# Kernel tuning notes

Measured on AMD Instinct MI355X. Metric: run time of the kernel, lower is better.

## Reference

```python
import jax, jax.numpy as jnp
import numpy as np

D_MODEL = 768
N_LAYER = 8
EXPAND = 2
D_INNER = EXPAND * D_MODEL          # 1536
HEADDIM = 64
NHEADS = D_INNER // HEADDIM         # 24
D_STATE = 128
D_CONV = 4
NGROUPS = 1
CONV_DIM = D_INNER + 2 * NGROUPS * D_STATE      # 1792
D_IN_PROJ = 2 * D_INNER + 2 * NGROUPS * D_STATE + NHEADS  # 3352
DIM_INP = 6
DIM_OUT = 5
BATCH = 4
SEQ = 2048
EPS = 1e-5


def rmsnorm(x, w):
    return x * jax.lax.rsqrt(jnp.mean(x * x, axis=-1, keepdims=True) + EPS) * w


def setup_inputs() -> dict:
    key = jax.random.key(0)
    ks = jax.random.split(key, 12)
    nrm = lambda k, shape, s=0.02: jax.random.normal(k, shape, jnp.float32) * s
    x = jax.random.normal(ks[0], (BATCH, SEQ, DIM_INP), jnp.float32)
    y = jax.random.normal(ks[1], (BATCH, SEQ, DIM_OUT), jnp.float32)
    W_emb = nrm(ks[2], (D_MODEL, DIM_INP))
    b_emb = jnp.zeros((D_MODEL,), jnp.float32)
    # stacked per-layer Mamba2 params
    W_in = nrm(ks[3], (N_LAYER, D_IN_PROJ, D_MODEL))
    conv_w = nrm(ks[4], (N_LAYER, CONV_DIM, D_CONV), 0.2)
    conv_b = jnp.zeros((N_LAYER, CONV_DIM), jnp.float32)
    dt0 = jax.random.uniform(ks[5], (N_LAYER, NHEADS), jnp.float32, 1e-3, 1e-1)
    dt_bias = jnp.log(jnp.expm1(dt0))  # inverse softplus of target dt
    A_log = jnp.log(jax.random.uniform(ks[6], (N_LAYER, NHEADS), jnp.float32, 1.0, 16.0))
    Dp = jnp.ones((N_LAYER, NHEADS), jnp.float32)
    norm_w = jnp.ones((N_LAYER, D_INNER), jnp.float32)     # gated RMSNorm inside Mamba2
    W_out = nrm(ks[7], (N_LAYER, D_MODEL, D_INNER))
    block_norm_w = jnp.ones((N_LAYER, D_MODEL), jnp.float32)  # prenorm RMSNorm per block
    norm_f_w = jnp.ones((D_MODEL,), jnp.float32)
    W_head = nrm(ks[8], (DIM_OUT, D_MODEL))
    return dict(x=x, y=y, W_emb=W_emb, b_emb=b_emb, W_in=W_in, conv_w=conv_w,
                conv_b=conv_b, dt_bias=dt_bias, A_log=A_log, Dp=Dp, norm_w=norm_w,
                W_out=W_out, block_norm_w=block_norm_w, norm_f_w=norm_f_w, W_head=W_head)


def _mamba2(u, W_in_l, conv_w_l, conv_b_l, dt_bias_l, A_log_l, D_l, norm_w_l, W_out_l):
    B, L, _ = u.shape
    zxbcdt = jnp.einsum('bld,ed->ble', u, W_in_l)  # [B,L,D_IN_PROJ]
    z = zxbcdt[..., :D_INNER]
    xBC = zxbcdt[..., D_INNER:D_INNER + CONV_DIM]
    dt = jax.nn.softplus(zxbcdt[..., D_INNER + CONV_DIM:] + dt_bias_l)  # [B,L,H]
    # causal depthwise conv1d, kernel D_CONV
    xp = jnp.pad(xBC, ((0, 0), (D_CONV - 1, 0), (0, 0)))
    xBC = sum(xp[:, k:k + L, :] * conv_w_l[:, k] for k in range(D_CONV)) + conv_b_l
    xBC = jax.nn.silu(xBC)
    xh = xBC[..., :D_INNER].reshape(B, L, NHEADS, HEADDIM)
    Bm = xBC[..., D_INNER:D_INNER + D_STATE]   # [B,L,N] (ngroups=1)
    Cm = xBC[..., D_INNER + D_STATE:]          # [B,L,N]
    A = -jnp.exp(A_log_l)                       # [H]
    decay = jnp.exp(dt * A)                     # [B,L,H]
    dtx = dt[..., None] * xh                    # [B,L,H,P]

    def step(h, inp):
        dec_t, dtx_t, B_t, C_t = inp            # [B,H],[B,H,P],[B,N],[B,N]
        h = h * dec_t[..., None, None] + dtx_t[..., None] * B_t[:, None, None, :]
        y_t = jnp.einsum('bhpn,bn->bhp', h, C_t)
        return h, y_t

    h0 = jnp.zeros((B, NHEADS, HEADDIM, D_STATE), u.dtype)
    _, ys = jax.lax.scan(step, h0, (decay.transpose(1, 0, 2), dtx.transpose(1, 0, 2, 3),
                                    Bm.transpose(1, 0, 2), Cm.transpose(1, 0, 2)))
    ys = ys.transpose(1, 0, 2, 3) + xh * D_l[None, None, :, None]  # skip term D*x
    yf = ys.reshape(B, L, D_INNER)
    yf = rmsnorm(yf * jax.nn.silu(z), norm_w_l)  # gated RMSNorm (norm_before_gate=False)
    return jnp.einsum('bld,ed->ble', yf, W_out_l)


def _forward(x, W_emb, b_emb, W_in, conv_w, conv_b, dt_bias, A_log, Dp, norm_w,
             W_out, block_norm_w, norm_f_w, W_head):
    h = jnp.einsum('bli,di->bld', x, W_emb) + b_emb
    res = jnp.zeros_like(h)

    def layer_step(carry, lp):
        h, res = carry
        Wi, cw, cb, dtb, Al, Dl, nw, Wo, bnw = lp
        res = h + res
        hn = rmsnorm(res, bnw)
        h = _mamba2(hn, Wi, cw, cb, dtb, Al, Dl, nw, Wo)
        return (h, res), None

    (h, res), _ = jax.lax.scan(layer_step, (h, res),
                               (W_in, conv_w, conv_b, dt_bias, A_log, Dp, norm_w, W_out, block_norm_w))
    res = h + res
    hn = rmsnorm(res, norm_f_w)
    return jnp.einsum('bld,od->blo', hn, W_head)


def reference(x, y, W_emb, b_emb, W_in, conv_w, conv_b, dt_bias, A_log, Dp, norm_w,
              W_out, block_norm_w, norm_f_w, W_head):
    out = _forward(x, W_emb, b_emb, W_in, conv_w, conv_b, dt_bias, A_log, Dp, norm_w,
                   W_out, block_norm_w, norm_f_w, W_head)
    loss = jnp.mean((out - y) ** 2)
    return out, loss
```

## Files before the change

### kernel.cpp

```cpp
#include <hip/hip_runtime.h>
#include <hip/hip_bf16.h>
#include <math.h>

#define BATCH 4
#define SEQ 2048
#define DMODEL 768
#define NLAYER 8
#define DINNER 1536
#define HEADDIM 64
#define NHEADS 24
#define DSTATE 128
#define CONVDIM 1792
#define DINPROJ 3352
#define NPAD 3456
#define NPADW 3584
#define ROWS (BATCH*SEQ)
#define EPS 1e-5f
#define QCH 128
#define NCH (SEQ/QCH)

typedef __bf16 bf16;
typedef bf16 bf16x8 __attribute__((ext_vector_type(8)));
typedef bf16 bf16x4 __attribute__((ext_vector_type(4)));
typedef float f32x4 __attribute__((ext_vector_type(4)));

#define GLD(src, dst) __builtin_amdgcn_global_load_lds( \
    (const __attribute__((address_space(1))) void*)(src), \
    (__attribute__((address_space(3))) void*)(dst), 16, 0, 0)

__device__ __forceinline__ void bar_sync() {
    asm volatile("" ::: "memory");
    __builtin_amdgcn_s_barrier();
    asm volatile("" ::: "memory");
}

__device__ __forceinline__ float fsilu(float x) { return x / (1.f + __expf(-x)); }

__global__ void k_embed(const float* __restrict__ x, const float* __restrict__ We,
                        const float* __restrict__ be, float* __restrict__ res) {
    int idx = blockIdx.x * 256 + threadIdx.x;
    int d0 = (idx % (DMODEL / 4)) * 4;
    int bl = idx / (DMODEL / 4);
    float xv[6];
#pragma unroll
    for (int i = 0; i < 6; ++i) xv[i] = x[bl * 6 + i];
    float4 o;
    float* op = &o.x;
#pragma unroll
    for (int j = 0; j < 4; ++j) {
        float acc = be[d0 + j];
#pragma unroll
        for (int i = 0; i < 6; ++i) acc += xv[i] * We[(d0 + j) * 6 + i];
        op[j] = acc;
    }
    *(float4*)(res + (long)bl * DMODEL + d0) = o;
}

__global__ __launch_bounds__(192) void k_rmsnorm(const float* __restrict__ res,
                                                 const float* __restrict__ w,
                                                 bf16* __restrict__ out) {
    __shared__ float sm[3];
    int r = blockIdx.x, tid = threadIdx.x;
    int d0 = tid * 4;
    float4 v = *(const float4*)(res + (long)r * DMODEL + d0);
    float ss = v.x * v.x + v.y * v.y + v.z * v.z + v.w * v.w;
#pragma unroll
    for (int off = 32; off; off >>= 1) ss += __shfl_down(ss, off, 64);
    if ((tid & 63) == 0) sm[tid >> 6] = ss;
    __syncthreads();
    float sc = rsqrtf((sm[0] + sm[1] + sm[2]) / (float)DMODEL + EPS);
    float4 wv = *(const float4*)(w + d0);
    bf16x4 o;
    o[0] = (bf16)(v.x * sc * wv.x);
    o[1] = (bf16)(v.y * sc * wv.y);
    o[2] = (bf16)(v.z * sc * wv.z);
    o[3] = (bf16)(v.w * sc * wv.w);
    *(bf16x4*)(out + (long)r * DMODEL + d0) = o;
}

__global__ void k_cvt_in(const float* __restrict__ src, bf16* __restrict__ dst) {
    long e = ((long)blockIdx.x * 256 + threadIdx.x) * 4;
    int l = (int)(e / (NPADW * DMODEL));
    long rem = e % (NPADW * DMODEL);
    int n = (int)(rem / DMODEL);
    int d = (int)(rem % DMODEL);
    bf16x4 o;
    if (n < DINPROJ) {
        float4 v = *(const float4*)(src + ((long)l * DINPROJ + n) * DMODEL + d);
        o[0] = (bf16)v.x; o[1] = (bf16)v.y; o[2] = (bf16)v.z; o[3] = (bf16)v.w;
    } else {
        o[0] = (bf16)0.f; o[1] = (bf16)0.f; o[2] = (bf16)0.f; o[3] = (bf16)0.f;
    }
    *(bf16x4*)(dst + e) = o;
}
__global__ void k_cvt_out(const float* __restrict__ src, bf16* __restrict__ dst) {
    long e = ((long)blockIdx.x * 256 + threadIdx.x) * 4;
    float4 v = *(const float4*)(src + e);
    bf16x4 o;
    o[0] = (bf16)v.x; o[1] = (bf16)v.y; o[2] = (bf16)v.z; o[3] = (bf16)v.w;
    *(bf16x4*)(dst + e) = o;
}

template <typename OT, int BM, int BN, int TH, bool ACC>
__global__ __launch_bounds__(TH) void k_gemm(const bf16* __restrict__ A, const bf16* __restrict__ B,
                                             OT* __restrict__ C, int K, int ldc, int Nact) {
    constexpr int NW  = TH / 64;
    constexpr int nWn = (BN / 64 < 4) ? BN / 64 : 4;
    constexpr int nWm = NW / nWn;
    constexpr int WMR = BM / nWm;
    constexpr int MI  = WMR / 16;
    constexpr int MH  = MI / 2;
    constexpr int NI  = 4;
    constexpr int RG  = TH / 8;
    constexpr int AG  = BM / RG;
    constexpr int BG  = BN / RG;
    __shared__ bf16 As[2][BM * 64];
    __shared__ bf16 Bs[2][BN * 64];
    const int tid = threadIdx.x;
    const int lane = tid & 63;
    const int w = tid >> 6;
    const int wm = w / nWn, wn = w % nWn;
    const long rowA0 = (long)blockIdx.x * BM;
    const long rowB0 = (long)blockIdx.y * BN;
    const int srow = tid >> 3;
    const int scol = ((tid & 7) ^ (srow & 7)) * 8;
    const bf16* Ab = A + rowA0 * K + scol;
    const bf16* Bb = B + rowB0 * K + scol;

    f32x4 acc[MI][NI];
    const f32x4 vz = {0.f, 0.f, 0.f, 0.f};
#pragma unroll
    for (int mi = 0; mi < MI; ++mi)
#pragma unroll
        for (int ni = 0; ni < NI; ++ni) acc[mi][ni] = vz;

    auto stage = [&](int buf, int kt) {
#pragma unroll
        for (int j = 0; j < AG; ++j)
            GLD(Ab + (long)(j * RG + srow) * K + kt, &As[buf][(j * TH + w * 64) * 8]);
#pragma unroll
        for (int j = 0; j < BG; ++j)
            GLD(Bb + (long)(j * RG + srow) * K + kt, &Bs[buf][(j * TH + w * 64) * 8]);
    };
    auto waitv = [&]() {
        if constexpr (AG + BG == 8) asm volatile("s_waitcnt vmcnt(8)" ::: "memory");
        else                        asm volatile("s_waitcnt vmcnt(6)" ::: "memory");
    };

    bf16x8 bfr[NI][2];
    bf16x8 af[MH][2];
    auto rd_bfr = [&](int buf) {
        const char* BsB = (const char*)Bs[buf];
#pragma unroll
        for (int ni = 0; ni < NI; ++ni)
#pragma unroll
            for (int ks = 0; ks < 2; ++ks) {
                int r = wn * 64 + ni * 16 + (lane & 15);
                bfr[ni][ks] = *(const bf16x8*)(BsB + r * 128 + ((ks * 64 + (lane >> 4) * 16) ^ ((r & 7) << 4)));
            }
    };
    auto rd_af = [&](int buf, int m0) {
        const char* AsB = (const char*)As[buf];
#pragma unroll
        for (int mi = 0; mi < MH; ++mi)
#pragma unroll
            for (int ks = 0; ks < 2; ++ks) {
                int r = wm * WMR + (m0 + mi) * 16 + (lane & 15);
                af[mi][ks] = *(const bf16x8*)(AsB + r * 128 + ((ks * 64 + (lane >> 4) * 16) ^ ((r & 7) << 4)));
            }
    };
    auto do_half = [&](int m0) {
#pragma unroll
        for (int mi = 0; mi < MH; ++mi)
#pragma unroll
            for (int ni = 0; ni < NI; ++ni)
#pragma unroll
                for (int ks = 0; ks < 2; ++ks)
                    acc[m0 + mi][ni] = __builtin_amdgcn_mfma_f32_16x16x32_bf16(af[mi][ks], bfr[ni][ks], acc[m0 + mi][ni], 0, 0, 0);
    };

    const int NT = K / 64;
    stage(0, 0);
    stage(1, 64);
    for (int t = 0; t < NT - 2; ++t) {
        waitv();
        bar_sync();
        rd_bfr(t & 1);
        rd_af(t & 1, 0);
        do_half(0);
        rd_af(t & 1, MH);
        asm volatile("s_waitcnt lgkmcnt(0)" ::: "memory");
        bar_sync();
        stage(t & 1, (t + 2) * 64);
        __builtin_amdgcn_sched_barrier(0);
        do_half(MH);
    }
    {
        waitv();
        bar_sync();
        rd_bfr((NT - 2) & 1);
        rd_af((NT - 2) & 1, 0);
        do_half(0);
        rd_af((NT - 2) & 1, MH);
        do_half(MH);
    }
    {
        asm volatile("s_waitcnt vmcnt(0)" ::: "memory");
        bar_sync();
        rd_bfr((NT - 1) & 1);
        rd_af((NT - 1) & 1, 0);
        do_half(0);
        rd_af((NT - 1) & 1, MH);
        do_half(MH);
    }

    const int crow = (lane >> 4) * 4;
    const int ccol = lane & 15;
#pragma unroll
    for (int mi = 0; mi < MI; ++mi)
#pragma unroll
        for (int ni = 0; ni < NI; ++ni) {
            long r0 = rowA0 + wm * WMR + mi * 16 + crow;
            long c0 = rowB0 + wn * 64 + ni * 16 + ccol;
            if ((int)c0 < Nact) {
#pragma unroll
                for (int j = 0; j < 4; ++j) {
                    if constexpr (ACC) C[(r0 + j) * ldc + c0] += (OT)acc[mi][ni][j];
                    else               C[(r0 + j) * ldc + c0]  = (OT)acc[mi][ni][j];
                }
            }
        }
}

__global__ void k_convBC(const bf16* __restrict__ zx, const float* __restrict__ cw,
                         const float* __restrict__ cb, bf16* __restrict__ bc) {
    int idx = blockIdx.x * 256 + threadIdx.x;
    int c8 = idx & 31; int blt = idx >> 5;
    int t = blt % SEQ;
    int ch = DINNER + c8 * 8;
    long bbase = (long)(blt - t) * NPAD;
    float cwa[8][4];
#pragma unroll
    for (int j = 0; j < 8; ++j) {
        float4 tv = *(const float4*)(cw + (ch + j) * 4);
        cwa[j][0] = tv.x; cwa[j][1] = tv.y; cwa[j][2] = tv.z; cwa[j][3] = tv.w;
    }
    float acc[8];
#pragma unroll
    for (int j = 0; j < 8; ++j) acc[j] = cb[ch + j];
#pragma unroll
    for (int k = 0; k < 4; ++k) {
        int tt = t + k - 3;
        if (tt >= 0) {
            bf16x8 v = *(const bf16x8*)(zx + bbase + (long)tt * NPAD + DINNER + ch);
#pragma unroll
            for (int j = 0; j < 8; ++j) acc[j] += (float)v[j] * cwa[j][k];
        }
    }
    bf16x8 o;
#pragma unroll
    for (int j = 0; j < 8; ++j) o[j] = (bf16)fsilu(acc[j]);
    *(bf16x8*)(bc + (long)blt * 256 + c8 * 8) = o;
}

__global__ __launch_bounds__(256) void k_prepL(const bf16* __restrict__ zx, const bf16* __restrict__ bc,
                                               const float* __restrict__ cw_l, const float* __restrict__ cb_l,
                                               const float* __restrict__ dt_bias_l,
                                               const float* __restrict__ Alog,
                                               float* __restrict__ Sarr, float* __restrict__ dtc,
                                               float* __restrict__ Pcb,
                                               bf16* __restrict__ XT, bf16* __restrict__ Lbuf) {
    __shared__ float S_lds[128], wl_lds[128], wtot[2];
    __shared__ bf16 Xs[136 * 64];
    __shared__ bf16 Xw[64 * 128];
    __shared__ bf16 Bt[128 * 128];
    int blk = blockIdx.x;
    int b = blk / (NHEADS * NCH);
    int r = blk % (NHEADS * NCH);
    int h = r / NCH;
    int c = r % NCH;
    int tid = threadIdx.x, lane = tid & 63, wid = tid >> 6;
    long brow0 = (long)b * SEQ + c * QCH;
#pragma unroll
    for (int i = 0; i < 5; ++i) {
        int base = i * 256 + wid * 64;
        if (base < 1048) {
            int idx = base + lane;
            long g = brow0 - 3 + (idx >> 3);
            if (g < 0) g = 0;
            if (g > (long)ROWS - 1) g = (long)ROWS - 1;
            GLD(zx + g * NPAD + DINNER + h * HEADDIM + (idx & 7) * 8,
                (char*)Xs + (long)base * 16);
        }
    }
    float ps = 0.f, dtv = 0.f;
    if (tid < 128) {
        float raw = (float)zx[(brow0 + tid) * NPAD + DINNER + CONVDIM + h] + dt_bias_l[h];
        dtv = (raw > 15.f) ? raw : log1pf(__expf(raw));
        float Ah = -__expf(Alog[h]);
        ps = dtv * Ah;
#pragma unroll
        for (int off = 1; off < 64; off <<= 1) {
            float o = __shfl_up(ps, off, 64);
            if ((tid & 63) >= off) ps += o;
        }
        if ((tid & 63) == 63) wtot[tid >> 6] = ps;
    }
    __syncthreads();
    if (tid < 128) {
        if (tid >= 64) ps += wtot[0];
        S_lds[tid] = ps;
    }
    __syncthreads();
    float Sl = S_lds[127];
    if (tid < 128) {
        wl_lds[tid] = __expf(Sl - ps) * dtv;
        Sarr[blk * QCH + tid] = ps;
        dtc[blk * QCH + tid] = dtv;
        if (tid == 127) Pcb[blk] = __expf(Sl);
    }
    __syncthreads();
    {
        int p = tid >> 2, q = tid & 3;
        float4 cwv = *(const float4*)(cw_l + (h * HEADDIM + p) * 4);
        float cbv = cb_l[h * HEADDIM + p];
        float cwa[4] = {cwv.x, cwv.y, cwv.z, cwv.w};
        char* xtb = (char*)XT + (((long)blk) << 14);
#pragma unroll
        for (int ub = 0; ub < 4; ++ub) {
            int u0 = q * 32 + ub * 8;
            bf16x8 vx, vw;
#pragma unroll
            for (int k = 0; k < 8; ++k) {
                int u = u0 + k;
                float a = cbv;
#pragma unroll
                for (int tt = 0; tt < 4; ++tt) {
                    if (c > 0 || u + tt >= 3)
                        a += (float)Xs[(u + tt) * 64 + p] * cwa[tt];
                }
                bf16 xb = (bf16)fsilu(a);
                vx[k] = xb;
                vw[k] = (bf16)((float)xb * wl_lds[u]);
            }
            long off = (long)((p * 256 + u0 * 2) ^ ((p & 7) << 4));
            *(bf16x8*)(xtb + off) = vx;
            *(bf16x8*)((char*)Xw + off) = vw;
        }
    }
#pragma unroll
    for (int nb = 0; nb < 2; ++nb) {
        __syncthreads();
#pragma unroll
        for (int i = 0; i < 4; ++i) {
            int idx = i * 256 + tid;
            GLD(bc + (brow0 + (idx >> 3)) * 256 + nb * 64 + (idx & 7) * 8,
                (char*)Xs + (i * 256 + wid * 64) * 16);
        }
        __syncthreads();
        int nl = tid >> 2, q = tid & 3;
        int n = nb * 64 + nl;
#pragma unroll
        for (int ub = 0; ub < 4; ++ub) {
            int u0 = q * 32 + ub * 8;
            bf16x8 v;
#pragma unroll
            for (int k = 0; k < 8; ++k) v[k] = Xs[(u0 + k) * 64 + nl];
            long off = (long)((n * 256 + u0 * 2) ^ ((n & 7) << 4));
            *(bf16x8*)((char*)Bt + off) = v;
        }
    }
    __syncthreads();
    f32x4 acc[4][2];
    const f32x4 vz = {0.f, 0.f, 0.f, 0.f};
#pragma unroll
    for (int mi = 0; mi < 4; ++mi)
#pragma unroll
        for (int ni = 0; ni < 2; ++ni) acc[mi][ni] = vz;
    const char* XwB = (const char*)Xw;
    const char* BtB = (const char*)Bt;
    __builtin_amdgcn_s_setprio(1);
#pragma unroll
    for (int ks = 0; ks < 4; ++ks) {
        bf16x8 af[4], bfr[2];
#pragma unroll
        for (int mi = 0; mi < 4; ++mi) {
            int pp = mi * 16 + (lane & 15);
            af[mi] = *(const bf16x8*)(XwB + ((pp * 256 + ks * 64 + (lane >> 4) * 16) ^ ((pp & 7) << 4)));
        }
#pragma unroll
        for (int ni = 0; ni < 2; ++ni) {
            int n = wid * 32 + ni * 16 + (lane & 15);
            bfr[ni] = *(const bf16x8*)(BtB + ((n * 256 + ks * 64 + (lane >> 4) * 16) ^ ((n & 7) << 4)));
        }
#pragma unroll
        for (int mi = 0; mi < 4; ++mi)
#pragma unroll
            for (int ni = 0; ni < 2; ++ni)
                acc[mi][ni] = __builtin_amdgcn_mfma_f32_16x16x32_bf16(af[mi], bfr[ni], acc[mi][ni], 0, 0, 0);
    }
    __builtin_amdgcn_s_setprio(0);
    char* lb = (char*)Lbuf + (((long)blk) << 14);
#pragma unroll
    for (int mi = 0; mi < 4; ++mi)
#pragma unroll
        for (int ni = 0; ni < 2; ++ni)
#pragma unroll
            for (int j = 0; j < 4; ++j) {
                int pp = mi * 16 + (lane >> 4) * 4 + j;
                int n = wid * 32 + ni * 16 + (lane & 15);
                *(bf16*)(lb + ((pp * 256 + n * 2) ^ ((pp & 7) << 4))) = (bf16)acc[mi][ni][j];
            }
}

__global__ __launch_bounds__(256) void k_scanB(bf16* __restrict__ Lbuf, const float* __restrict__ Pc) {
    int bh = blockIdx.x >> 2;
    int q = blockIdx.x & 3;
    int off = (q * 256 + threadIdx.x) * 8;
    long base = ((long)bh * NCH) << 13;
    float s[8] = {0.f};
#pragma unroll
    for (int c = 0; c < NCH; ++c) {
        bf16* p = Lbuf + base + ((long)c << 13) + off;
        bf16x8 L = *(bf16x8*)p;
        bf16x8 I;
#pragma unroll
        for (int k = 0; k < 8; ++k) I[k] = (bf16)s[k];
        float P = Pc[bh * NCH + c];
#pragma unroll
        for (int k = 0; k < 8; ++k) s[k] = P * s[k] + (float)L[k];
        *(bf16x8*)p = I;
    }
}

__global__ __launch_bounds__(512) void k_chunkY(const bf16* __restrict__ bc,
                                                const float* __restrict__ Sarr, const float* __restrict__ dtc,
                                                const float* __restrict__ Dp,
                                                const bf16* __restrict__ XT, const bf16* __restrict__ Lbuf,
                                                bf16* __restrict__ ysb) {
    __shared__ bf16 Cs[128 * 128];
    __shared__ bf16 Bs[128 * 128];
    __shared__ float S_lds[128], dt_lds[128];
    int blk = blockIdx.x;
    int b = blk / (NHEADS * NCH);
    int r = blk % (NHEADS * NCH);
    int h = r / NCH;
    int c = r % NCH;
    int tid = threadIdx.x, lane = tid & 63, wid = tid >> 6;
    long brow0 = (long)b * SEQ + c * QCH;
    const char* bcB = (const char*)bc;
#pragma unroll
    for (int i = 0; i < 4; ++i) {
        int trow = i * 32 + wid * 4 + (lane >> 4);
        int blk16 = lane & 15;
        const char* rp = bcB + (brow0 + trow) * 512;
        int sb = (blk16 ^ (trow & 7)) << 4;
        GLD(rp + 256 + sb, (char*)Cs + (i * 32 + wid * 4) * 256);
        GLD(rp + sb,       (char*)Bs + (i * 32 + wid * 4) * 256);
    }
    if (tid < 128) { S_lds[tid] = Sarr[blk * QCH + tid]; dt_lds[tid] = dtc[blk * QCH + tid]; }
    float Dh = Dp[h];
    const char* xtG = (const char*)XT + (((long)blk) << 14);
    const char* ibG = (const char*)Lbuf + (((long)blk) << 14);
    asm volatile("s_waitcnt vmcnt(0) lgkmcnt(0)" ::: "memory");
    bar_sync();
    const char* CsB = (const char*)Cs;
    char* BsB = (char*)Bs;
    const f32x4 vz = {0.f, 0.f, 0.f, 0.f};
    int wmG = wid >> 2, wnG = wid & 3;
    f32x4 accg[4][2];
#pragma unroll
    for (int mi = 0; mi < 4; ++mi)
#pragma unroll
        for (int ni = 0; ni < 2; ++ni) accg[mi][ni] = vz;
#pragma unroll
    for (int ks = 0; ks < 4; ++ks) {
        bf16x8 af[4], bfr[2];
#pragma unroll
        for (int mi = 0; mi < 4; ++mi) {
            int t = wmG * 64 + mi * 16 + (lane & 15);
            af[mi] = *(const bf16x8*)(CsB + ((t * 256 + ks * 64 + (lane >> 4) * 16) ^ ((t & 7) << 4)));
        }
#pragma unroll
        for (int ni = 0; ni < 2; ++ni) {
            int u = wnG * 32 + ni * 16 + (lane & 15);
            bfr[ni] = *(const bf16x8*)(BsB + ((u * 256 + ks * 64 + (lane >> 4) * 16) ^ ((u & 7) << 4)));
        }
#pragma unroll
        for (int mi = 0; mi < 4; ++mi)
#pragma unroll
            for (int ni = 0; ni < 2; ++ni)
                accg[mi][ni] = __builtin_amdgcn_mfma_f32_16x16x32_bf16(af[mi], bfr[ni], accg[mi][ni], 0, 0, 0);
    }
    bar_sync();
#pragma unroll
    for (int mi = 0; mi < 4; ++mi) {
#pragma unroll
        for (int j = 0; j < 4; ++j) {
            int t = wmG * 64 + mi * 16 + (lane >> 4) * 4 + j;
            float St = S_lds[t];
#pragma unroll
            for (int ni = 0; ni < 2; ++ni) {
                int u = wnG * 32 + ni * 16 + (lane & 15);
                float v = 0.f;
                if (u <= t) v = accg[mi][ni][j] * __expf(St - S_lds[u]) * dt_lds[u];
                *(bf16*)(BsB + ((t * 256 + u * 2) ^ ((t & 7) << 4))) = (bf16)v;
            }
        }
    }
    asm volatile("s_waitcnt lgkmcnt(0)" ::: "memory");
    bar_sync();
    int wmY = wid >> 1, wnY = wid & 1;
    f32x4 accy[2][2];
#pragma unroll
    for (int mi = 0; mi < 2; ++mi)
#pragma unroll
        for (int ni = 0; ni < 2; ++ni) accy[mi][ni] = vz;
#pragma unroll
    for (int ks = 0; ks < 4; ++ks) {
        bf16x8 af[2], bfr[2];
#pragma unroll
        for (int mi = 0; mi < 2; ++mi) {
            int t = wmY * 32 + mi * 16 + (lane & 15);
            af[mi] = *(const bf16x8*)(CsB + ((t * 256 + ks * 64 + (lane >> 4) * 16) ^ ((t & 7) << 4)));
        }
#pragma unroll
        for (int ni = 0; ni < 2; ++ni) {
            int pp = wnY * 32 + ni * 16 + (lane & 15);
            bfr[ni] = *(const bf16x8*)(ibG + ((pp * 256 + ks * 64 + (lane >> 4) * 16) ^ ((pp & 7) << 4)));
        }
#pragma unroll
        for (int mi = 0; mi < 2; ++mi)
#pragma unroll
            for (int ni = 0; ni < 2; ++ni)
                accy[mi][ni] = __builtin_amdgcn_mfma_f32_16x16x32_bf16(af[mi], bfr[ni], accy[mi][ni], 0, 0, 0);
    }
#pragma unroll
    for (int mi = 0; mi < 2; ++mi)
#pragma unroll
        for (int j = 0; j < 4; ++j) {
            int t = wmY * 32 + mi * 16 + (lane >> 4) * 4 + j;
            float e = __expf(S_lds[t]);
#pragma unroll
            for (int ni = 0; ni < 2; ++ni) accy[mi][ni][j] *= e;
        }
#pragma unroll
    for (int ks = 0; ks < 4; ++ks) {
        bf16x8 af[2], bfr[2];
#pragma unroll
        for (int mi = 0; mi < 2; ++mi) {
            int t = wmY * 32 + mi * 16 + (lane & 15);
            af[mi] = *(const bf16x8*)(BsB + ((t * 256 + ks * 64 + (lane >> 4) * 16) ^ ((t & 7) << 4)));
        }
#pragma unroll
        for (int ni = 0; ni < 2; ++ni) {
            int pp = wnY * 32 + ni * 16 + (lane & 15);
            bfr[ni] = *(const bf16x8*)(xtG + ((pp * 256 + ks * 64 + (lane >> 4) * 16) ^ ((pp & 7) << 4)));
        }
#pragma unroll
        for (int mi = 0; mi < 2; ++mi)
#pragma unroll
            for (int ni = 0; ni < 2; ++ni)
                accy[mi][ni] = __builtin_amdgcn_mfma_f32_16x16x32_bf16(af[mi], bfr[ni], accy[mi][ni], 0, 0, 0);
    }
#pragma unroll
    for (int mi = 0; mi < 2; ++mi)
#pragma unroll
        for (int ni = 0; ni < 2; ++ni)
#pragma unroll
            for (int j = 0; j < 4; ++j) {
                int t = wmY * 32 + mi * 16 + (lane >> 4) * 4 + j;
                int pp = wnY * 32 + ni * 16 + (lane & 15);
                float xv = (float)*(const bf16*)(xtG + ((pp * 256 + t * 2) ^ ((pp & 7) << 4)));
                ysb[(brow0 + t) * DINNER + h * HEADDIM + pp] = (bf16)(accy[mi][ni][j] + Dh * xv);
            }
}

__global__ __launch_bounds__(192) void k_gated(const bf16* __restrict__ ys, const bf16* __restrict__ zx,
                                               const float* __restrict__ w, bf16* __restrict__ out) {
    __shared__ float sm[3];
    int r = blockIdx.x, tid = threadIdx.x;
    int d0 = tid * 8;
    bf16x8 yv = *(const bf16x8*)(ys + (long)r * DINNER + d0);
    bf16x8 zv = *(const bf16x8*)(zx + (long)r * NPAD + d0);
    float v[8]; float ss = 0.f;
#pragma unroll
    for (int j = 0; j < 8; ++j) {
        float t = (float)yv[j] * fsilu((float)zv[j]);
        v[j] = t; ss += t * t;
    }
#pragma unroll
    for (int off = 32; off; off >>= 1) ss += __shfl_down(ss, off, 64);
    if ((tid & 63) == 0) sm[tid >> 6] = ss;
    __syncthreads();
    float sc = rsqrtf((sm[0] + sm[1] + sm[2]) / (float)DINNER + EPS);
    float4 w0 = *(const float4*)(w + d0);
    float4 w1 = *(const float4*)(w + d0 + 4);
    float wa[8] = {w0.x, w0.y, w0.z, w0.w, w1.x, w1.y, w1.z, w1.w};
    bf16x8 o;
#pragma unroll
    for (int j = 0; j < 8; ++j) o[j] = (bf16)(v[j] * sc * wa[j]);
    *(bf16x8*)(out + (long)r * DINNER + d0) = o;
}

__global__ __launch_bounds__(256) void k_head(const bf16* __restrict__ hn, const float* __restrict__ Wh,
                                              const float* __restrict__ y, float* __restrict__ out,
                                              float* __restrict__ loss) {
    __shared__ float sl[4];
    int tid = threadIdx.x, lane = tid & 63, wid = tid >> 6;
    float wv[5][12];
#pragma unroll
    for (int o = 0; o < 5; ++o)
#pragma unroll
        for (int j = 0; j < 12; ++j) wv[o][j] = Wh[o * DMODEL + lane * 12 + j];
    float lsum = 0.f;
#pragma unroll
    for (int rr = 0; rr < 8; ++rr) {
        long r = (long)blockIdx.x * 32 + wid * 8 + rr;
        const bf16* hp = hn + r * DMODEL + lane * 12;
        float hv[12];
#pragma unroll
        for (int q = 0; q < 3; ++q) {
            bf16x4 v4 = *(const bf16x4*)(hp + q * 4);
#pragma unroll
            for (int j = 0; j < 4; ++j) hv[q * 4 + j] = (float)v4[j];
        }
        float acc[5];
#pragma unroll
        for (int o = 0; o < 5; ++o) {
            float a = 0.f;
#pragma unroll
            for (int j = 0; j < 12; ++j) a += hv[j] * wv[o][j];
            acc[o] = a;
        }
#pragma unroll
        for (int o = 0; o < 5; ++o)
#pragma unroll
            for (int m = 32; m; m >>= 1) acc[o] += __shfl_xor(acc[o], m, 64);
        if (lane == 0) {
#pragma unroll
            for (int o = 0; o < 5; ++o) {
                out[r * 5 + o] = acc[o];
                float d = acc[o] - y[r * 5 + o];
                lsum += d * d;
            }
        }
    }
    if (lane == 0) sl[wid] = lsum;
    __syncthreads();
    if (tid == 0) atomicAdd(loss, (sl[0] + sl[1] + sl[2] + sl[3]) * (1.f / ((float)ROWS * 5.f)));
}

extern "C" void kernel_launch(void* const* d_in, const int* in_sizes, int n_in,
                              void* d_out, int out_size, void* d_ws, size_t ws_size,
                              hipStream_t stream) {
    const float* x      = (const float*)d_in[0];
    const float* y      = (const float*)d_in[1];
    const float* W_emb  = (const float*)d_in[2];
    const float* b_emb  = (const float*)d_in[3];
    const float* W_in   = (const float*)d_in[4];
    const float* conv_w = (const float*)d_in[5];
    const float* conv_b = (const float*)d_in[6];
    const float* dt_bias= (const float*)d_in[7];
    const float* A_log  = (const float*)d_in[8];
    const float* Dp     = (const float*)d_in[9];
    const float* norm_w = (const float*)d_in[10];
    const float* W_out  = (const float*)d_in[11];
    const float* bnw    = (const float*)d_in[12];
    const float* nfw    = (const float*)d_in[13];
    const float* W_head = (const float*)d_in[14];

    char* ws = (char*)d_ws;
    float* res  = (float*)ws;  ws += (size_t)ROWS * DMODEL * 4;
    bf16*  Lbuf = (bf16*)ws;   ws += (size_t)BATCH * NHEADS * NCH * 8192 * 2;
    bf16*  hnb  = (bf16*)ws;   ws += (size_t)ROWS * DMODEL * 2;
    bf16*  zx   = (bf16*)ws;   ws += (size_t)ROWS * NPAD * 2;
    bf16*  bc   = (bf16*)ws;   ws += (size_t)ROWS * 256 * 2;
    bf16*  ysb  = (bf16*)ws;   ws += (size_t)ROWS * DINNER * 2;
    bf16*  yfb  = (bf16*)ws;   ws += (size_t)ROWS * DINNER * 2;
    bf16*  Wib  = (bf16*)ws;   ws += (size_t)NLAYER * NPADW * DMODEL * 2;
    bf16*  Wob  = (bf16*)ws;   ws += (size_t)NLAYER * DMODEL * DINNER * 2;
    float* Pcb  = (float*)ws;  ws += (size_t)BATCH * NHEADS * NCH * 4;
    float* Sarr = (float*)ws;  ws += (size_t)BATCH * NHEADS * NCH * QCH * 4;
    float* dtc  = (float*)ws;  ws += (size_t)BATCH * NHEADS * NCH * QCH * 4;
    bf16*  XT   = (bf16*)ws;   ws += (size_t)BATCH * NHEADS * NCH * 8192 * 2;

    float* out_p  = (float*)d_out;
    float* loss_p = out_p + (size_t)ROWS * 5;

    hipMemsetAsync(loss_p, 0, 4, stream);
    k_embed<<<ROWS * (DMODEL / 4) / 256, 256, 0, stream>>>(x, W_emb, b_emb, res);
    k_cvt_in<<<NLAYER * NPADW * DMODEL / 4 / 256, 256, 0, stream>>>(W_in, Wib);
    k_cvt_out<<<NLAYER * DMODEL * DINNER / 4 / 256, 256, 0, stream>>>(W_out, Wob);

    const int NBHC = BATCH * NHEADS * NCH;
    for (int l = 0; l < NLAYER; ++l) {
        const float* cw_l = conv_w + (size_t)l * CONVDIM * 4;
        const float* cb_l = conv_b + (size_t)l * CONVDIM;
        k_rmsnorm<<<ROWS, 192, 0, stream>>>(res, bnw + l * DMODEL, hnb);
        dim3 g1(ROWS / 256, NPADW / 256);
        k_gemm<bf16, 256, 256, 512, false><<<g1, 512, 0, stream>>>(hnb, Wib + (size_t)l * NPADW * DMODEL, zx, DMODEL, NPAD, NPAD);
        k_convBC<<<ROWS * 32 / 256, 256, 0, stream>>>(zx, cw_l, cb_l, bc);
        k_prepL<<<NBHC, 256, 0, stream>>>(zx, bc, cw_l, cb_l, dt_bias + l * NHEADS, A_log + l * NHEADS,
                                          Sarr, dtc, Pcb, XT, Lbuf);
        k_scanB<<<BATCH * NHEADS * 4, 256, 0, stream>>>(Lbuf, Pcb);
        k_chunkY<<<NBHC, 512, 0, stream>>>(bc, Sarr, dtc, Dp + l * NHEADS, XT, Lbuf, ysb);
        k_gated<<<ROWS, 192, 0, stream>>>(ysb, zx, norm_w + l * DINNER, yfb);
        dim3 g2(ROWS / 128, DMODEL / 64);
        k_gemm<float, 128, 64, 256, true><<<g2, 256, 0, stream>>>(yfb, Wob + (size_t)l * DMODEL * DINNER, res, DINNER, DMODEL, DMODEL);
    }

    k_rmsnorm<<<ROWS, 192, 0, stream>>>(res, nfw, hnb);
    k_head<<<256, 256, 0, stream>>>(hnb, W_head, y, out_p, loss_p);
}
```

Measured before the change: 1.668 ms.

## Restructure GEMM main loop to single-stage prefetch and pairwise A-fragment reads

```diff
diff --git a/kernel.cpp b/kernel.cpp
--- a/kernel.cpp
+++ b/kernel.cpp
@@ -109,7 +109,6 @@
     constexpr int nWm = NW / nWn;
     constexpr int WMR = BM / nWm;
     constexpr int MI  = WMR / 16;
-    constexpr int MH  = MI / 2;
     constexpr int NI  = 4;
     constexpr int RG  = TH / 8;
     constexpr int AG  = BM / RG;
@@ -148,7 +147,7 @@
     };
 
     bf16x8 bfr[NI][2];
-    bf16x8 af[MH][2];
+    bf16x8 af[2][2];
     auto rd_bfr = [&](int buf) {
         const char* BsB = (const char*)Bs[buf];
 #pragma unroll
@@ -159,19 +158,19 @@
                 bfr[ni][ks] = *(const bf16x8*)(BsB + r * 128 + ((ks * 64 + (lane >> 4) * 16) ^ ((r & 7) << 4)));
             }
     };
-    auto rd_af = [&](int buf, int m0) {
+    auto rd_af2 = [&](int buf, int m0) {
         const char* AsB = (const char*)As[buf];
 #pragma unroll
-        for (int mi = 0; mi < MH; ++mi)
+        for (int mi = 0; mi < 2; ++mi)
 #pragma unroll
             for (int ks = 0; ks < 2; ++ks) {
                 int r = wm * WMR + (m0 + mi) * 16 + (lane & 15);
                 af[mi][ks] = *(const bf16x8*)(AsB + r * 128 + ((ks * 64 + (lane >> 4) * 16) ^ ((r & 7) << 4)));
             }
     };
-    auto do_half = [&](int m0) {
-#pragma unroll
-        for (int mi = 0; mi < MH; ++mi)
+    auto do_pair = [&](int m0) {
+#pragma unroll
+        for (int mi = 0; mi < 2; ++mi)
 #pragma unroll
             for (int ni = 0; ni < NI; ++ni)
 #pragma unroll
@@ -181,37 +180,22 @@
 
     const int NT = K / 64;
     stage(0, 0);
-    stage(1, 64);
-    for (int t = 0; t < NT - 2; ++t) {
-        waitv();
+    for (int t = 0; t < NT; ++t) {
         bar_sync();
-        rd_bfr(t & 1);
-        rd_af(t & 1, 0);
-        do_half(0);
-        rd_af(t & 1, MH);
-        asm volatile("s_waitcnt lgkmcnt(0)" ::: "memory");
+        if (t + 1 < NT) {
+            stage((t + 1) & 1, (t + 1) * 64);
+            waitv();
+        } else {
+            asm volatile("s_waitcnt vmcnt(0)" ::: "memory");
+        }
         bar_sync();
-        stage(t & 1, (t + 2) * 64);
-        __builtin_amdgcn_sched_barrier(0);
-        do_half(MH);
-    }
-    {
-        waitv();
-        bar_sync();
-        rd_bfr((NT - 2) & 1);
-        rd_af((NT - 2) & 1, 0);
-        do_half(0);
-        rd_af((NT - 2) & 1, MH);
-        do_half(MH);
-    }
-    {
-        asm volatile("s_waitcnt vmcnt(0)" ::: "memory");
-        bar_sync();
-        rd_bfr((NT - 1) & 1);
-        rd_af((NT - 1) & 1, 0);
-        do_half(0);
-        rd_af((NT - 1) & 1, MH);
-        do_half(MH);
+        const int buf = t & 1;
+        rd_bfr(buf);
+#pragma unroll
+        for (int c = 0; c < MI; c += 2) {
+            rd_af2(buf, c);
+            do_pair(c);
+        }
     }
 
     const int crow = (lane >> 4) * 4;
```

Result: no change. 1.680 ms (+0.7%).
